# Optimization experiments

Hardware: AMD Instinct MI355X
Metric: run time of the kernel (lower is better)

Reference implementation:

```python
import jax, jax.numpy as jnp
import numpy as np

H, W = 2048, 2048          # frame size (cascade_size)
CS = 227                   # classifier_size
K = 16                     # max components classified per frame (fixed budget)
NC = 4                     # num_classes
THRESH = 0.5               # binarization threshold
MIN_SIZE = 64              # min component pixel count
CC_ITERS = 64              # label-propagation iterations for connected components


def _conv(x, w, stride=1, padding='SAME'):
    return jax.lax.conv_general_dilated(x, w, (stride, stride), padding,
                                        dimension_numbers=('NCHW', 'OIHW', 'NCHW'))


def _cascade(x, w1, w2, w3):
    # stand-in for Unet_plus(1,1): full-res segmentation head -> sigmoid mask
    h = jax.nn.relu(_conv(x, w1))
    h = jax.nn.relu(_conv(h, w2))
    return jax.nn.sigmoid(_conv(h, w3))   # [1,1,H,W]


def _classifier(roi, cw1, cw2, fc):
    # stand-in for CompactNet: roi [B,1,CS,CS] -> logits [B,NC]
    h = jax.nn.relu(_conv(roi, cw1, stride=4, padding='VALID'))
    h = jax.nn.relu(_conv(h, cw2, stride=2, padding='VALID'))
    g = h.mean(axis=(2, 3))               # global average pool -> [B,32]
    return g @ fc


def _connected_components(mask):
    # GPU-style min-index label propagation, 4-connectivity; background label = H*W
    BIG = H * W
    lab = jnp.where(mask, jnp.arange(BIG, dtype=jnp.int32).reshape(H, W), BIG)
    def step(_, lab):
        p = jnp.pad(lab, 1, constant_values=BIG)
        nmin = jnp.minimum(jnp.minimum(p[:-2, 1:-1], p[2:, 1:-1]),
                           jnp.minimum(p[1:-1, :-2], p[1:-1, 2:]))
        return jnp.where(mask, jnp.minimum(lab, nmin), BIG)
    return jax.lax.fori_loop(0, CC_ITERS, step, lab)


def _roi_resize(img, y0, y1, x0, x1):
    # bilinear warp of axis-aligned box [y0:y1, x0:x1] to CS x CS
    t = jnp.linspace(0.0, 1.0, CS)
    gy = y0.astype(jnp.float32) + t * (y1 - y0).astype(jnp.float32)
    gx = x0.astype(jnp.float32) + t * (x1 - x0).astype(jnp.float32)
    yf = jnp.clip(jnp.floor(gy).astype(jnp.int32), 0, H - 2)
    xf = jnp.clip(jnp.floor(gx).astype(jnp.int32), 0, W - 2)
    fy = (gy - yf)[:, None]
    fx = (gx - xf)[None, :]
    v00 = img[yf[:, None], xf[None, :]]
    v01 = img[yf[:, None], (xf + 1)[None, :]]
    v10 = img[(yf + 1)[:, None], xf[None, :]]
    v11 = img[(yf + 1)[:, None], (xf + 1)[None, :]]
    return (1 - fy) * ((1 - fx) * v00 + fx * v01) + fy * ((1 - fx) * v10 + fx * v11)


def _detect(x, w1, w2, w3, cw1, cw2, fc):
    pred_mask = _cascade(x, w1, w2, w3)[0, 0]          # [H,W]
    img = x[0, 0]
    mask = pred_mask > THRESH
    lab = jax.lax.stop_gradient(_connected_components(mask))
    counts = jnp.zeros(H * W + 1, jnp.int32).at[lab.ravel()].add(1)
    counts = counts.at[H * W].set(0)                   # drop background
    cnts, lids = jax.lax.top_k(counts, K)              # K largest components

    def per_comp(lid, cnt):
        cm = lab == lid                                # [H,W] component mask
        valid = (cnt >= MIN_SIZE)
        rowany = cm.any(axis=1)
        colany = cm.any(axis=0)
        y0 = jnp.argmax(rowany); y1 = H - 1 - jnp.argmax(rowany[::-1])
        x0 = jnp.argmax(colany); x1 = W - 1 - jnp.argmax(colany[::-1])
        roi = _roi_resize(img, y0, y1, x0, x1)         # [CS,CS] warped crop
        logits = _classifier(roi[None, None], cw1, cw2, fc)[0]
        return logits, cm, valid

    logits, cms, valids = jax.vmap(per_comp)(lids, cnts)   # [K,NC],[K,H,W],[K]
    return logits, cms, valids


def reference(x, w1, w2, w3, cw1, cw2, fc):
    logits, cms, valids = _detect(x, w1, w2, w3, cw1, cw2, fc)
    onehot = jax.nn.one_hot(jnp.argmax(logits, axis=1), NC) * valids[:, None]
    masks = jnp.einsum('kc,khw->chw', onehot, cms.astype(jnp.float32))
    return jnp.clip(masks, 0.0, 1.0)                   # [NC,H,W] per-class masks


def setup_inputs():
    key = jax.random.key(0)
    ks = jax.random.split(key, 7)
    def nrm(k, shape, fan_in):
        return jax.random.normal(k, shape, jnp.float32) / np.sqrt(fan_in).astype(np.float32)
    return {
        'x':   jax.random.normal(ks[0], (1, 1, H, W), jnp.float32),
        'w1':  nrm(ks[1], (32, 1, 3, 3), 9),
        'w2':  nrm(ks[2], (32, 32, 3, 3), 288),
        'w3':  nrm(ks[3], (1, 32, 1, 1), 32),
        'cw1': nrm(ks[4], (16, 1, 7, 7), 49),
        'cw2': nrm(ks[5], (32, 16, 3, 3), 144),
        'fc':  nrm(ks[6], (32, NC), 32),
    }
```

## Files before the change

### kernel.cpp

```cpp
#include <hip/hip_runtime.h>

#define HH 2048
#define WW 2048
#define HWTOT 4194304
#define BIGL 4194304
#define CSZ 227
#define NCLS 4
#define MINSZ 64
#define TF 1.1920928955078125e-7f
#define EPSB 5e-3f
#define LISTCAP 4000000

#define OFF_LABA 0u
#define OFF_LABB (1u<<24)
#define OFF_H1C  ((1u<<24) + 3538944u)
#define OFF_H2C  ((1u<<24) + 7077888u)
#define OFF_CAND ((1u<<24) + 9437184u)
#define OFF_CAND16 ((1u<<24) + 9437184u + 524288u)
#define OFF_COUNTS (2u<<24)
#define OFF_W2R  ((3u<<24) + 4096u)
#define OFF_LIST ((3u<<24) + 131072u)

typedef __attribute__((ext_vector_type(8))) short bf16x8;
typedef __attribute__((ext_vector_type(4))) float f32x4;
typedef unsigned int uint;
typedef unsigned short ushort;
typedef unsigned long long u64;

struct Meta {
  int lids[16];
  int valid[16];
  int cls[16];
  int bby0[16], bby1[16], bbx0[16], bbx1[16];
};

__device__ __forceinline__ ushort f2bf(float f) {
  uint u = __float_as_uint(f);
  u += 0x7fffu + ((u >> 16) & 1u);
  return (ushort)(u >> 16);
}
__device__ __forceinline__ float bf2f(ushort h) {
  return __uint_as_float(((uint)h) << 16);
}

#define HSWZ(px, g) ((px) * 32 + ((((g) ^ ((px) & 3))) << 3))

__global__ __launch_bounds__(256) void prep_kernel(const float* __restrict__ w2,
                                                   ushort* __restrict__ wfrag) {
  int i = blockIdx.x * 256 + threadIdx.x;
  if (i >= 18432) return;
  int fid = i >> 9, within = i & 511;
  int lane = within >> 3, j = within & 7;
  int tap = fid >> 2, m = (fid >> 1) & 1, p = fid & 1;
  int row = lane & 15, kgrp = lane >> 4;
  int ci = kgrp * 8 + j, oc = m * 16 + row;
  float w = w2[oc * 288 + ci * 9 + tap];
  ushort hb = f2bf(w);
  ushort val = hb;
  if (p) { float lof = w - bf2f(hb); val = f2bf(lof); }
  wfrag[i] = val;
}

__global__ __launch_bounds__(256) void cascade_kernel(
    const float* __restrict__ x, const float* __restrict__ w1,
    const ushort* __restrict__ wfrag, const float* __restrict__ w3,
    int* __restrict__ lab, int* __restrict__ list, int* __restrict__ list_count) {
  __shared__ float xs[12][36];
  __shared__ __align__(16) short hbuf[2][10880];

  const int tid = threadIdx.x;
  const int ox = blockIdx.x * 32, oy = blockIdx.y * 8;

  for (int i = tid; i < 432; i += 256) {
    int r = i / 36, c = i - r * 36;
    int gy = oy - 2 + r, gx = ox - 2 + c;
    float v = 0.f;
    if ((unsigned)gy < (unsigned)HH && (unsigned)gx < (unsigned)WW) v = x[gy * WW + gx];
    xs[r][c] = v;
  }
  __syncthreads();

  for (int px = tid; px < 340; px += 256) {
    const int hr = px / 34, hc = px - hr * 34;
    const int gy = oy - 1 + hr, gx = ox - 1 + hc;
    const bool inimg = ((unsigned)gy < (unsigned)HH) && ((unsigned)gx < (unsigned)WW);
    float a9[9];
#pragma unroll
    for (int du = 0; du < 3; ++du)
#pragma unroll
      for (int dv = 0; dv < 3; ++dv) a9[du * 3 + dv] = xs[hr + du][hc + dv];
#pragma unroll 1
    for (int g = 0; g < 4; ++g) {
      float sv[8];
#pragma unroll
      for (int cj = 0; cj < 8; ++cj) {
        const int ci = g * 8 + cj;
        float s = 0.f;
#pragma unroll
        for (int t = 0; t < 9; ++t) s = fmaf(a9[t], w1[ci * 9 + t], s);
        sv[cj] = inimg ? fmaxf(s, 0.f) : 0.f;
      }
      uint hp[4], lp[4];
#pragma unroll
      for (int q = 0; q < 4; ++q) {
        float s0 = sv[2 * q], s1 = sv[2 * q + 1];
        uint h2u;
        asm("v_cvt_pk_bf16_f32 %0, %1, %2" : "=v"(h2u) : "v"(s0), "v"(s1));
        float h0 = __uint_as_float(h2u << 16);
        float h1 = __uint_as_float(h2u & 0xffff0000u);
        uint l2u;
        asm("v_cvt_pk_bf16_f32 %0, %1, %2" : "=v"(l2u) : "v"(s0 - h0), "v"(s1 - h1));
        hp[q] = h2u; lp[q] = l2u;
      }
      *(int4*)&hbuf[0][HSWZ(px, g)] = make_int4(hp[0], hp[1], hp[2], hp[3]);
      *(int4*)&hbuf[1][HSWZ(px, g)] = make_int4(lp[0], lp[1], lp[2], lp[3]);
    }
  }
  __syncthreads();

  const int wv = tid >> 6, lane = tid & 63;
  const int col = lane & 15, kg = lane >> 4;
  const f32x4 zero4 = {0.f, 0.f, 0.f, 0.f};
  f32x4 acc[4][2];
#pragma unroll
  for (int i = 0; i < 4; ++i) { acc[i][0] = zero4; acc[i][1] = zero4; }

  const int4* wf4 = (const int4*)wfrag;
#pragma unroll 3
  for (int tap = 0; tap < 9; ++tap) {
    const int ty = tap / 3, tx = tap - ty * 3;
    bf16x8 a[2][2];
#pragma unroll
    for (int m = 0; m < 2; ++m)
#pragma unroll
      for (int p = 0; p < 2; ++p)
        a[m][p] = __builtin_bit_cast(bf16x8, wf4[(tap * 4 + m * 2 + p) * 64 + lane]);
#pragma unroll
    for (int ni = 0; ni < 4; ++ni) {
      const int nt = wv * 4 + ni;
      const int px = ((nt >> 1) + ty) * 34 + (nt & 1) * 16 + tx + col;
      bf16x8 bh = __builtin_bit_cast(bf16x8, *(const int4*)&hbuf[0][HSWZ(px, kg)]);
      bf16x8 bl = __builtin_bit_cast(bf16x8, *(const int4*)&hbuf[1][HSWZ(px, kg)]);
      acc[ni][0] = __builtin_amdgcn_mfma_f32_16x16x32_bf16(a[0][0], bh, acc[ni][0], 0, 0, 0);
      acc[ni][1] = __builtin_amdgcn_mfma_f32_16x16x32_bf16(a[1][0], bh, acc[ni][1], 0, 0, 0);
      acc[ni][0] = __builtin_amdgcn_mfma_f32_16x16x32_bf16(a[0][1], bh, acc[ni][0], 0, 0, 0);
      acc[ni][1] = __builtin_amdgcn_mfma_f32_16x16x32_bf16(a[1][1], bh, acc[ni][1], 0, 0, 0);
      acc[ni][0] = __builtin_amdgcn_mfma_f32_16x16x32_bf16(a[0][0], bl, acc[ni][0], 0, 0, 0);
      acc[ni][1] = __builtin_amdgcn_mfma_f32_16x16x32_bf16(a[1][0], bl, acc[ni][1], 0, 0, 0);
    }
  }

#pragma unroll 1
  for (int ni = 0; ni < 4; ++ni) {
    const int nt = wv * 4 + ni;
    float z = 0.f;
#pragma unroll
    for (int m = 0; m < 2; ++m)
#pragma unroll
      for (int r = 0; r < 4; ++r)
        z = fmaf(w3[m * 16 + kg * 4 + r], fmaxf(acc[ni][m][r], 0.f), z);
    z += __shfl_xor(z, 16);
    z += __shfl_xor(z, 32);
    const int gy = oy + (nt >> 1), gx = ox + (nt & 1) * 16 + col;
    const int p = gy * WW + gx;
    const bool act = lane < 16;
    if (act) lab[p] = (z > TF) ? p : BIGL;
    bool need = act && (fabsf(z - TF) < EPSB);
    unsigned long long mms = __ballot(need);
    if (mms) {
      int cnt = __popcll(mms);
      int prefix = __popcll(mms & ((1ull << lane) - 1ull));
      int basei = 0;
      if (need && prefix == 0) basei = atomicAdd(list_count, cnt);
      int srcl = __ffsll((long long)mms) - 1;
      basei = __shfl(basei, srcl);
      if (need && basei + prefix < LISTCAP) list[basei + prefix] = p;
    }
  }
}

__global__ __launch_bounds__(256) void recheck_kernel(
    const float* __restrict__ x, const float* __restrict__ w1,
    const float* __restrict__ w2, const float* __restrict__ w3,
    const int* __restrict__ list, const int* __restrict__ list_count,
    int* __restrict__ lab) {
  int n = *list_count;
  if (n > LISTCAP) n = LISTCAP;
  const int half = threadIdx.x & 1;
  for (int i = (blockIdx.x * 256 + threadIdx.x) >> 1; i < n; i += (2048 * 256) >> 1) {
    int p = list[i];
    int py = p >> 11, px = p & 2047;
    float xv[5][5];
#pragma unroll
    for (int u = 0; u < 5; ++u)
#pragma unroll
      for (int v = 0; v < 5; ++v) {
        int gy = py - 2 + u, gx = px - 2 + v;
        xv[u][v] = ((unsigned)gy < (unsigned)HH && (unsigned)gx < (unsigned)WW)
                       ? x[gy * WW + gx] : 0.f;
      }
    double acc2[32];
#pragma unroll
    for (int j = 0; j < 32; ++j) acc2[j] = 0.0;
    const int ci0 = half * 16;
#pragma unroll 1
    for (int ci = ci0; ci < ci0 + 16; ++ci) {
      float h1v[3][3];
#pragma unroll
      for (int u = 0; u < 3; ++u)
#pragma unroll
        for (int v = 0; v < 3; ++v) {
          int gy = py - 1 + u, gx = px - 1 + v;
          float s = 0.f;
#pragma unroll
          for (int t9 = 0; t9 < 9; ++t9)
            s = fmaf(xv[u + t9 / 3][v + t9 % 3], w1[ci * 9 + t9], s);
          bool inb = ((unsigned)gy < (unsigned)HH) && ((unsigned)gx < (unsigned)WW);
          h1v[u][v] = (inb && (s > 0.f)) ? s : 0.f;
        }
#pragma unroll
      for (int dy = 0; dy < 3; ++dy)
#pragma unroll
        for (int dx = 0; dx < 3; ++dx) {
          double hd = (double)h1v[dy][dx];
#pragma unroll
          for (int j = 0; j < 32; ++j)
            acc2[j] = fma(hd, (double)w2[j * 288 + ci * 9 + dy * 3 + dx], acc2[j]);
        }
    }
    double zz = 0.0;
#pragma unroll
    for (int j = 0; j < 32; ++j) {
      double other = __shfl_xor(acc2[j], 1);
      double tot = (half == 0) ? (acc2[j] + other) : (other + acc2[j]);
      zz = fma((double)w3[j], tot > 0.0 ? tot : 0.0, zz);
    }
    if (half == 0) lab[p] = (zz > 1.1920928955078125e-7) ? p : BIGL;
  }
}

__global__ __launch_bounds__(256) void cc16_kernel(const int* __restrict__ in,
                                                   int* __restrict__ out) {
  __shared__ __align__(16) int edgeL[24][100];
  __shared__ __align__(16) int edgeR[24][100];
  __shared__ __align__(16) int4 vtop[8][25];
  __shared__ __align__(16) int4 vbot[8][25];
  const int tid = threadIdx.x;
  const int bx = blockIdx.x & 31, by = blockIdx.x >> 5;
  const int ox0 = bx * 64 - 16, oy0 = by * 64 - 16;
  const bool act = tid < 192;
  const int g = tid % 24, s = tid / 24;
  const int gx = ox0 + g * 4;
  const bool colin = ((unsigned)gx < (unsigned)WW);
  int4 c[12];
#pragma unroll
  for (int r = 0; r < 12; ++r) c[r] = make_int4(BIGL, BIGL, BIGL, BIGL);
  if (act && colin) {
#pragma unroll
    for (int r = 0; r < 12; ++r) {
      int gy = oy0 + s * 12 + r;
      if ((unsigned)gy < (unsigned)HH) c[r] = *(const int4*)(in + gy * WW + gx);
    }
  }
#pragma unroll 1
  for (int step = 0; step < 16; ++step) {
    if (act) {
      *(int4*)&edgeL[g][s * 12 + 0] = make_int4(c[0].x, c[1].x, c[2].x, c[3].x);
      *(int4*)&edgeL[g][s * 12 + 4] = make_int4(c[4].x, c[5].x, c[6].x, c[7].x);
      *(int4*)&edgeL[g][s * 12 + 8] = make_int4(c[8].x, c[9].x, c[10].x, c[11].x);
      *(int4*)&edgeR[g][s * 12 + 0] = make_int4(c[0].w, c[1].w, c[2].w, c[3].w);
      *(int4*)&edgeR[g][s * 12 + 4] = make_int4(c[4].w, c[5].w, c[6].w, c[7].w);
      *(int4*)&edgeR[g][s * 12 + 8] = make_int4(c[8].w, c[9].w, c[10].w, c[11].w);
      vtop[s][g] = c[0];
      vbot[s][g] = c[11];
    }
    __syncthreads();
    if (act) {
      int lf[12], rt[12];
      if (g > 0) {
        int4 a0 = *(const int4*)&edgeR[g - 1][s * 12 + 0];
        int4 a1 = *(const int4*)&edgeR[g - 1][s * 12 + 4];
        int4 a2 = *(const int4*)&edgeR[g - 1][s * 12 + 8];
        lf[0] = a0.x; lf[1] = a0.y; lf[2] = a0.z; lf[3] = a0.w;
        lf[4] = a1.x; lf[5] = a1.y; lf[6] = a1.z; lf[7] = a1.w;
        lf[8] = a2.x; lf[9] = a2.y; lf[10] = a2.z; lf[11] = a2.w;
      } else {
#pragma unroll
        for (int r = 0; r < 12; ++r) lf[r] = BIGL;
      }
      if (g < 23) {
        int4 a0 = *(const int4*)&edgeL[g + 1][s * 12 + 0];
        int4 a1 = *(const int4*)&edgeL[g + 1][s * 12 + 4];
        int4 a2 = *(const int4*)&edgeL[g + 1][s * 12 + 8];
        rt[0] = a0.x; rt[1] = a0.y; rt[2] = a0.z; rt[3] = a0.w;
        rt[4] = a1.x; rt[5] = a1.y; rt[6] = a1.z; rt[7] = a1.w;
        rt[8] = a2.x; rt[9] = a2.y; rt[10] = a2.z; rt[11] = a2.w;
      } else {
#pragma unroll
        for (int r = 0; r < 12; ++r) rt[r] = BIGL;
      }
      int4 prev = (s > 0) ? vbot[s - 1][g] : make_int4(BIGL, BIGL, BIGL, BIGL);
      int4 dnlast = (s < 7) ? vtop[s + 1][g] : make_int4(BIGL, BIGL, BIGL, BIGL);
#pragma unroll
      for (int r = 0; r < 12; ++r) {
        int4 cur = c[r];
        int4 d = (r < 11) ? c[r + 1] : dnlast;
        int4 nr;
        nr.x = (cur.x == BIGL) ? BIGL : min(min(cur.x, cur.y), min(min(prev.x, d.x), lf[r]));
        nr.y = (cur.y == BIGL) ? BIGL : min(min(cur.y, min(cur.x, cur.z)), min(prev.y, d.y));
        nr.z = (cur.z == BIGL) ? BIGL : min(min(cur.z, min(cur.y, cur.w)), min(prev.z, d.z));
        nr.w = (cur.w == BIGL) ? BIGL : min(min(cur.w, min(cur.z, rt[r])), min(prev.w, d.w));
        c[r] = nr;
        prev = cur;
      }
    }
    __syncthreads();
  }
  if (act && g >= 4 && g < 20) {
#pragma unroll
    for (int r = 0; r < 12; ++r) {
      int row = s * 12 + r;
      if (row >= 16 && row < 80) {
        int gy = oy0 + row;
        *(int4*)(out + gy * WW + gx) = c[r];
      }
    }
  }
}

__global__ __launch_bounds__(256) void hist_kernel(const int* __restrict__ lab,
                                                   int* __restrict__ counts) {
  __shared__ int hkey[4096];
  __shared__ int hval[4096];
  int tid = threadIdx.x;
  for (int i = tid; i < 4096; i += 256) { hkey[i] = -1; hval[i] = 0; }
  __syncthreads();
  int t = blockIdx.x * 256 + tid;
  int p = t * 8;
  int4 a = *(const int4*)(lab + p), b = *(const int4*)(lab + p + 4);
  int v[8] = {a.x, a.y, a.z, a.w, b.x, b.y, b.z, b.w};
  int prev = -1, run = 0;
#pragma unroll
  for (int j = 0; j < 8; ++j) {
    int l = v[j];
    if (l == prev) { run++; continue; }
    if (prev >= 0 && prev != BIGL) {
      unsigned hh = (((unsigned)prev * 2654435761u) >> 20) & 4095u;
      for (;;) {
        int k = atomicCAS(&hkey[hh], -1, prev);
        if (k == -1 || k == prev) { atomicAdd(&hval[hh], run); break; }
        hh = (hh + 1) & 4095u;
      }
    }
    prev = l; run = 1;
  }
  if (prev >= 0 && prev != BIGL) {
    unsigned hh = (((unsigned)prev * 2654435761u) >> 20) & 4095u;
    for (;;) {
      int k = atomicCAS(&hkey[hh], -1, prev);
      if (k == -1 || k == prev) { atomicAdd(&hval[hh], run); break; }
      hh = (hh + 1) & 4095u;
    }
  }
  __syncthreads();
  for (int i = tid; i < 4096; i += 256)
    if (hkey[i] >= 0) atomicAdd(&counts[hkey[i]], hval[i]);
}

__global__ __launch_bounds__(256) void cand_kernel(const int* __restrict__ counts,
                                                   int2* __restrict__ cand,
                                                   int* __restrict__ cand_count) {
  int i = blockIdx.x * 256 + threadIdx.x;
  int lane = threadIdx.x & 63;
  int c = (i < HWTOT) ? counts[i] : 0;
  bool hit = (c >= MINSZ);
  unsigned long long m = __ballot(hit);
  if (m) {
    int cnt = __popcll(m);
    int prefix = __popcll(m & ((1ull << lane) - 1ull));
    int base = 0;
    if (hit && prefix == 0) base = atomicAdd(cand_count, cnt);
    int srcl = __ffsll((long long)m) - 1;
    base = __shfl(base, srcl);
    if (hit && base + prefix < 65536) cand[base + prefix] = make_int2(c, i);
  }
}

__global__ __launch_bounds__(256) void top16a_kernel(const int2* __restrict__ cand,
                                                     const int* __restrict__ cand_count,
                                                     u64* __restrict__ cand16) {
  __shared__ u64 skey[256];
  int tid = threadIdx.x;
  int n = *cand_count;
  if (n > 65536) n = 65536;
  u64 prev = ~0ull;
  for (int r = 0; r < 16; ++r) {
    u64 best = 0ull;
    for (int i = blockIdx.x * 256 + tid; i < n; i += 32 * 256) {
      int2 cc = cand[i];
      u64 key = ((u64)(unsigned)cc.x << 32) | (unsigned)(BIGL - cc.y);
      if (key < prev && key > best) best = key;
    }
    skey[tid] = best;
    __syncthreads();
    for (int st = 128; st > 0; st >>= 1) {
      if (tid < st && skey[tid + st] > skey[tid]) skey[tid] = skey[tid + st];
      __syncthreads();
    }
    u64 blockbest = skey[0];
    if (tid == 0) cand16[blockIdx.x * 16 + r] = blockbest;
    prev = blockbest;
    __syncthreads();
  }
}

__global__ __launch_bounds__(256) void top16b_kernel(const u64* __restrict__ cand16,
                                                     Meta* __restrict__ meta) {
  __shared__ u64 skey[256];
  int tid = threadIdx.x;
  u64 k0 = cand16[tid], k1 = cand16[tid + 256];
  u64 prev = ~0ull;
  for (int r = 0; r < 16; ++r) {
    u64 best = 0ull;
    if (k0 < prev && k0 > best) best = k0;
    if (k1 < prev && k1 > best) best = k1;
    skey[tid] = best;
    __syncthreads();
    for (int st = 128; st > 0; st >>= 1) {
      if (tid < st && skey[tid + st] > skey[tid]) skey[tid] = skey[tid + st];
      __syncthreads();
    }
    u64 blockbest = skey[0];
    if (tid == 0) {
      if (blockbest > 0ull) {
        meta->lids[r] = BIGL - (int)(blockbest & 0xffffffffull);
        meta->valid[r] = 1;
      } else {
        meta->lids[r] = -1;
        meta->valid[r] = 0;
      }
    }
    prev = blockbest;
    __syncthreads();
  }
  if (tid < 16) {
    meta->bby0[tid] = HH; meta->bby1[tid] = -1;
    meta->bbx0[tid] = WW; meta->bbx1[tid] = -1;
    meta->cls[tid] = 0;
  }
}

__global__ __launch_bounds__(256) void bbox_kernel(const int* __restrict__ lab,
                                                   Meta* __restrict__ meta) {
  __shared__ int lid_s[16];
  __shared__ int by0[16], by1[16], bx0[16], bx1[16];
  int tid = threadIdx.x;
  if (tid < 16) {
    lid_s[tid] = meta->lids[tid];
    by0[tid] = HH; by1[tid] = -1; bx0[tid] = WW; bx1[tid] = -1;
  }
  __syncthreads();
  int t = blockIdx.x * 256 + tid;
  int p = t * 8;
  int y = p >> 11, xbase = p & 2047;
  int4 a = *(const int4*)(lab + p), b = *(const int4*)(lab + p + 4);
  int v[8] = {a.x, a.y, a.z, a.w, b.x, b.y, b.z, b.w};
  int prev = BIGL, kprev = -1, xs = 0, xe = 0;
#pragma unroll
  for (int j = 0; j < 8; ++j) {
    int l = v[j];
    if (l == prev) { xe = xbase + j; continue; }
    if (kprev >= 0) {
      atomicMin(&by0[kprev], y); atomicMax(&by1[kprev], y);
      atomicMin(&bx0[kprev], xs); atomicMax(&bx1[kprev], xe);
    }
    prev = l; xs = xe = xbase + j; kprev = -1;
    if (l != BIGL) {
      for (int k = 0; k < 16; ++k)
        if (lid_s[k] == l) { kprev = k; break; }
    }
  }
  if (kprev >= 0) {
    atomicMin(&by0[kprev], y); atomicMax(&by1[kprev], y);
    atomicMin(&bx0[kprev], xs); atomicMax(&bx1[kprev], xe);
  }
  __syncthreads();
  if (tid < 16 && by1[tid] >= 0) {
    atomicMin(&meta->bby0[tid], by0[tid]); atomicMax(&meta->bby1[tid], by1[tid]);
    atomicMin(&meta->bbx0[tid], bx0[tid]); atomicMax(&meta->bbx1[tid], bx1[tid]);
  }
}

__global__ __launch_bounds__(256) void cconv1_kernel(const float* __restrict__ img,
                                                     const float* __restrict__ cw1,
                                                     const Meta* __restrict__ meta,
                                                     float* __restrict__ h1c) {
  int k = blockIdx.y, oy = blockIdx.x;
  if (!meta->valid[k]) return;
  __shared__ float srow[7][CSZ];
  float y0 = (float)meta->bby0[k], y1 = (float)meta->bby1[k];
  float x0 = (float)meta->bbx0[k], x1 = (float)meta->bbx1[k];
  for (int idx = threadIdx.x; idx < 7 * CSZ; idx += 256) {
    int rr = idx / CSZ, j = idx - rr * CSZ;
    int i = oy * 4 + rr;
    float ti = (float)i / 226.f, tj = (float)j / 226.f;
    float gy = y0 + ti * (y1 - y0);
    float gx = x0 + tj * (x1 - x0);
    int yf = (int)floorf(gy); yf = yf < 0 ? 0 : (yf > HH - 2 ? HH - 2 : yf);
    int xf = (int)floorf(gx); xf = xf < 0 ? 0 : (xf > WW - 2 ? WW - 2 : xf);
    float fy = gy - (float)yf, fx = gx - (float)xf;
    const float* r0 = img + yf * WW + xf;
    float v00 = r0[0], v01 = r0[1], v10 = r0[WW], v11 = r0[WW + 1];
    srow[rr][j] = (1.f - fy) * ((1.f - fx) * v00 + fx * v01) +
                  fy * ((1.f - fx) * v10 + fx * v11);
  }
  __syncthreads();
  for (int idx = threadIdx.x; idx < 16 * 56; idx += 256) {
    int ch = idx / 56, ox = idx - ch * 56;
    const float* wp = cw1 + ch * 49;
    float s = 0.f;
#pragma unroll
    for (int dy = 0; dy < 7; ++dy)
#pragma unroll
      for (int dx = 0; dx < 7; ++dx)
        s += srow[dy][ox * 4 + dx] * wp[dy * 7 + dx];
    h1c[((k * 16 + ch) * 56 + oy) * 56 + ox] = s > 0.f ? s : 0.f;
  }
}

__global__ __launch_bounds__(256) void cconv2_kernel(const float* __restrict__ h1c,
                                                     const float* __restrict__ cw2,
                                                     const Meta* __restrict__ meta,
                                                     float* __restrict__ h2c) {
  int k = blockIdx.y, oy = blockIdx.x;
  if (!meta->valid[k]) return;
  for (int idx = threadIdx.x; idx < 32 * 27; idx += 256) {
    int ch = idx / 27, ox = idx - ch * 27;
    float s = 0.f;
    for (int ci = 0; ci < 16; ++ci) {
      const float* hp = h1c + ((k * 16 + ci) * 56 + oy * 2) * 56 + ox * 2;
      const float* wp = cw2 + (ch * 16 + ci) * 9;
#pragma unroll
      for (int dy = 0; dy < 3; ++dy)
#pragma unroll
        for (int dx = 0; dx < 3; ++dx) s += hp[dy * 56 + dx] * wp[dy * 3 + dx];
    }
    h2c[((k * 32 + ch) * 27 + oy) * 27 + ox] = s > 0.f ? s : 0.f;
  }
}

__global__ __launch_bounds__(256) void poolfc_kernel(const float* __restrict__ h2c,
                                                     const float* __restrict__ fc,
                                                     Meta* __restrict__ meta) {
  int k = blockIdx.x;
  if (!meta->valid[k]) return;
  __shared__ float sums[8][32];
  int tid = threadIdx.x;
  int c = tid & 31, part = tid >> 5;
  float s = 0.f;
  const float* hp = h2c + (k * 32 + c) * 729;
  for (int j = part; j < 729; j += 8) s += hp[j];
  sums[part][c] = s;
  __syncthreads();
  if (tid < 32) {
    float g = 0.f;
#pragma unroll
    for (int p2 = 0; p2 < 8; ++p2) g += sums[p2][tid];
    sums[0][tid] = g / 729.f;
  }
  __syncthreads();
  if (tid == 0) {
    float best = -1e30f;
    int bi = 0;
    for (int j = 0; j < NCLS; ++j) {
      float lg = 0.f;
      for (int c2 = 0; c2 < 32; ++c2) lg += sums[0][c2] * fc[c2 * NCLS + j];
      if (lg > best) { best = lg; bi = j; }
    }
    meta->cls[k] = bi;
  }
}

__global__ __launch_bounds__(256) void final_kernel(const float* labf,
                                                    const Meta* __restrict__ meta,
                                                    float* out) {
  __shared__ int lid_s[16];
  __shared__ int cls_s[16];
  int tid = threadIdx.x;
  if (tid < 16) {
    lid_s[tid] = meta->valid[tid] ? meta->lids[tid] : -1;
    cls_s[tid] = meta->cls[tid];
  }
  __syncthreads();
  int t = blockIdx.x * 256 + tid;
  int p = t * 4;
  float4 lf = *(const float4*)(labf + p);
  int l4[4] = {__float_as_int(lf.x), __float_as_int(lf.y), __float_as_int(lf.z),
               __float_as_int(lf.w)};
  int cj[4];
#pragma unroll
  for (int j = 0; j < 4; ++j) {
    cj[j] = -1;
    int l = l4[j];
    if (l != BIGL) {
      for (int k = 0; k < 16; ++k)
        if (lid_s[k] == l) { cj[j] = cls_s[k]; break; }
    }
  }
#pragma unroll
  for (int c = 0; c < 4; ++c) {
    float4 w4 = make_float4(cj[0] == c ? 1.f : 0.f, cj[1] == c ? 1.f : 0.f,
                            cj[2] == c ? 1.f : 0.f, cj[3] == c ? 1.f : 0.f);
    *(float4*)(out + (size_t)c * HWTOT + p) = w4;
  }
}

extern "C" void kernel_launch(void* const* d_in, const int* in_sizes, int n_in,
                              void* d_out, int out_size, void* d_ws, size_t ws_size,
                              hipStream_t stream) {
  const float* x = (const float*)d_in[0];
  const float* w1 = (const float*)d_in[1];
  const float* w2 = (const float*)d_in[2];
  const float* w3 = (const float*)d_in[3];
  const float* cw1 = (const float*)d_in[4];
  const float* cw2 = (const float*)d_in[5];
  const float* fc = (const float*)d_in[6];

  char* base = (char*)d_out;
  int* lab_a = (int*)(base + OFF_LABA);
  int* lab_b = (int*)(base + OFF_LABB);
  float* h1c = (float*)(base + OFF_H1C);
  float* h2c = (float*)(base + OFF_H2C);
  int2* cand = (int2*)(base + OFF_CAND);
  u64* cand16 = (u64*)(base + OFF_CAND16);
  int* counts = (int*)(base + OFF_COUNTS);
  ushort* wfrag = (ushort*)(base + OFF_W2R);
  int* list = (int*)(base + OFF_LIST);
  int* cand_count = (int*)d_ws;
  int* list_count = (int*)((char*)d_ws + 64);
  Meta* meta = (Meta*)((char*)d_ws + 256);

  hipMemsetAsync(counts, 0, (size_t)(HWTOT + 1) * sizeof(int), stream);
  hipMemsetAsync(d_ws, 0, 128, stream);

  prep_kernel<<<72, 256, 0, stream>>>(w2, wfrag);
  cascade_kernel<<<dim3(64, 256), 256, 0, stream>>>(x, w1, wfrag, w3, lab_a, list, list_count);
  recheck_kernel<<<2048, 256, 0, stream>>>(x, w1, w2, w3, list, list_count, lab_a);

  for (int l = 0; l < 4; ++l) {
    const int* src = (l & 1) ? lab_b : lab_a;
    int* dst = (l & 1) ? lab_a : lab_b;
    cc16_kernel<<<1024, 256, 0, stream>>>(src, dst);
  }

  hist_kernel<<<2048, 256, 0, stream>>>(lab_a, counts);
  cand_kernel<<<16384, 256, 0, stream>>>(counts, cand, cand_count);
  top16a_kernel<<<32, 256, 0, stream>>>(cand, cand_count, cand16);
  top16b_kernel<<<1, 256, 0, stream>>>(cand16, meta);
  bbox_kernel<<<2048, 256, 0, stream>>>(lab_a, meta);
  cconv1_kernel<<<dim3(56, 16), 256, 0, stream>>>(x, cw1, meta, h1c);
  cconv2_kernel<<<dim3(27, 16), 256, 0, stream>>>(h1c, cw2, meta, h2c);
  poolfc_kernel<<<16, 256, 0, stream>>>(h2c, fc, meta);
  final_kernel<<<4096, 256, 0, stream>>>((const float*)d_out, meta, (float*)d_out);
}
```

Measured before the change: 662.6 us.

## Fuse label histogram into last CC pass and split recheck across four lanes

The final connected-components pass now builds the per-label shared-memory hash histogram from its register-resident labels, so the separate hist kernel and its full re-read of the label map are gone. The recheck kernel splits the 32 output channels across four lanes instead of two, each computing all 32 input channels with 8 double accumulators. The results are combined with two xor-shuffles. The workspace memset is folded into prep_kernel. This trades one global pass and one launch for more shared memory and an extra sync in the last CC kernel, and for redundant layer-1 compute in recheck.

```diff
diff --git a/kernel.cpp b/kernel.cpp
--- a/kernel.cpp
+++ b/kernel.cpp
@@ -34,6 +34,13 @@
   int bby0[16], bby1[16], bbx0[16], bbx1[16];
 };
 
+struct CCShared {
+  int edgeL[24][100];
+  int edgeR[24][100];
+  int4 vtop[8][25];
+  int4 vbot[8][25];
+};
+
 __device__ __forceinline__ ushort f2bf(float f) {
   uint u = __float_as_uint(f);
   u += 0x7fffu + ((u >> 16) & 1u);
@@ -46,7 +53,9 @@
 #define HSWZ(px, g) ((px) * 32 + ((((g) ^ ((px) & 3))) << 3))
 
 __global__ __launch_bounds__(256) void prep_kernel(const float* __restrict__ w2,
-                                                   ushort* __restrict__ wfrag) {
+                                                   ushort* __restrict__ wfrag,
+                                                   int* __restrict__ ws) {
+  if (blockIdx.x == 0 && threadIdx.x < 32) ws[threadIdx.x] = 0;
   int i = blockIdx.x * 256 + threadIdx.x;
   if (i >= 18432) return;
   int fid = i >> 9, within = i & 511;
@@ -186,9 +195,9 @@
     int* __restrict__ lab) {
   int n = *list_count;
   if (n > LISTCAP) n = LISTCAP;
-  const int half = threadIdx.x & 1;
-  for (int i = (blockIdx.x * 256 + threadIdx.x) >> 1; i < n; i += (2048 * 256) >> 1) {
-    int p = list[i];
+  const int jg = threadIdx.x & 3;
+  for (int q = (blockIdx.x * 256 + threadIdx.x) >> 2; q < n; q += (2048 * 256) >> 2) {
+    int p = list[q];
     int py = p >> 11, px = p & 2047;
     float xv[5][5];
 #pragma unroll
@@ -199,12 +208,11 @@
         xv[u][v] = ((unsigned)gy < (unsigned)HH && (unsigned)gx < (unsigned)WW)
                        ? x[gy * WW + gx] : 0.f;
       }
-    double acc2[32];
-#pragma unroll
-    for (int j = 0; j < 32; ++j) acc2[j] = 0.0;
-    const int ci0 = half * 16;
+    double acc2[8];
+#pragma unroll
+    for (int j = 0; j < 8; ++j) acc2[j] = 0.0;
 #pragma unroll 1
-    for (int ci = ci0; ci < ci0 + 16; ++ci) {
+    for (int ci = 0; ci < 32; ++ci) {
       float h1v[3][3];
 #pragma unroll
       for (int u = 0; u < 3; ++u)
@@ -224,27 +232,36 @@
         for (int dx = 0; dx < 3; ++dx) {
           double hd = (double)h1v[dy][dx];
 #pragma unroll
-          for (int j = 0; j < 32; ++j)
-            acc2[j] = fma(hd, (double)w2[j * 288 + ci * 9 + dy * 3 + dx], acc2[j]);
+          for (int j = 0; j < 8; ++j)
+            acc2[j] = fma(hd, (double)w2[(jg * 8 + j) * 288 + ci * 9 + dy * 3 + dx],
+                          acc2[j]);
         }
     }
     double zz = 0.0;
 #pragma unroll
-    for (int j = 0; j < 32; ++j) {
-      double other = __shfl_xor(acc2[j], 1);
-      double tot = (half == 0) ? (acc2[j] + other) : (other + acc2[j]);
-      zz = fma((double)w3[j], tot > 0.0 ? tot : 0.0, zz);
-    }
-    if (half == 0) lab[p] = (zz > 1.1920928955078125e-7) ? p : BIGL;
-  }
-}
-
+    for (int j = 0; j < 8; ++j)
+      zz = fma((double)w3[jg * 8 + j], acc2[j] > 0.0 ? acc2[j] : 0.0, zz);
+    zz += __shfl_xor(zz, 1);
+    zz += __shfl_xor(zz, 2);
+    if (jg == 0) lab[p] = (zz > 1.1920928955078125e-7) ? p : BIGL;
+  }
+}
+
+__device__ __forceinline__ void hist_add(int* hkey, int* hval, int label, int run) {
+  unsigned hh = (((unsigned)label * 2654435761u) >> 20) & 4095u;
+  for (;;) {
+    int k = atomicCAS(&hkey[hh], -1, label);
+    if (k == -1 || k == label) { atomicAdd(&hval[hh], run); break; }
+    hh = (hh + 1) & 4095u;
+  }
+}
+
+template <int DOHIST>
 __global__ __launch_bounds__(256) void cc16_kernel(const int* __restrict__ in,
-                                                   int* __restrict__ out) {
-  __shared__ __align__(16) int edgeL[24][100];
-  __shared__ __align__(16) int edgeR[24][100];
-  __shared__ __align__(16) int4 vtop[8][25];
-  __shared__ __align__(16) int4 vbot[8][25];
+                                                   int* __restrict__ out,
+                                                   int* __restrict__ counts) {
+  __shared__ __align__(16) char smem[32768];
+  CCShared* S = (CCShared*)smem;
   const int tid = threadIdx.x;
   const int bx = blockIdx.x & 31, by = blockIdx.x >> 5;
   const int ox0 = bx * 64 - 16, oy0 = by * 64 - 16;
@@ -265,22 +282,22 @@
 #pragma unroll 1
   for (int step = 0; step < 16; ++step) {
     if (act) {
-      *(int4*)&edgeL[g][s * 12 + 0] = make_int4(c[0].x, c[1].x, c[2].x, c[3].x);
-      *(int4*)&edgeL[g][s * 12 + 4] = make_int4(c[4].x, c[5].x, c[6].x, c[7].x);
-      *(int4*)&edgeL[g][s * 12 + 8] = make_int4(c[8].x, c[9].x, c[10].x, c[11].x);
-      *(int4*)&edgeR[g][s * 12 + 0] = make_int4(c[0].w, c[1].w, c[2].w, c[3].w);
-      *(int4*)&edgeR[g][s * 12 + 4] = make_int4(c[4].w, c[5].w, c[6].w, c[7].w);
-      *(int4*)&edgeR[g][s * 12 + 8] = make_int4(c[8].w, c[9].w, c[10].w, c[11].w);
-      vtop[s][g] = c[0];
-      vbot[s][g] = c[11];
+      *(int4*)&S->edgeL[g][s * 12 + 0] = make_int4(c[0].x, c[1].x, c[2].x, c[3].x);
+      *(int4*)&S->edgeL[g][s * 12 + 4] = make_int4(c[4].x, c[5].x, c[6].x, c[7].x);
+      *(int4*)&S->edgeL[g][s * 12 + 8] = make_int4(c[8].x, c[9].x, c[10].x, c[11].x);
+      *(int4*)&S->edgeR[g][s * 12 + 0] = make_int4(c[0].w, c[1].w, c[2].w, c[3].w);
+      *(int4*)&S->edgeR[g][s * 12 + 4] = make_int4(c[4].w, c[5].w, c[6].w, c[7].w);
+      *(int4*)&S->edgeR[g][s * 12 + 8] = make_int4(c[8].w, c[9].w, c[10].w, c[11].w);
+      S->vtop[s][g] = c[0];
+      S->vbot[s][g] = c[11];
     }
     __syncthreads();
     if (act) {
       int lf[12], rt[12];
       if (g > 0) {
-        int4 a0 = *(const int4*)&edgeR[g - 1][s * 12 + 0];
-        int4 a1 = *(const int4*)&edgeR[g - 1][s * 12 + 4];
-        int4 a2 = *(const int4*)&edgeR[g - 1][s * 12 + 8];
+        int4 a0 = *(const int4*)&S->edgeR[g - 1][s * 12 + 0];
+        int4 a1 = *(const int4*)&S->edgeR[g - 1][s * 12 + 4];
+        int4 a2 = *(const int4*)&S->edgeR[g - 1][s * 12 + 8];
         lf[0] = a0.x; lf[1] = a0.y; lf[2] = a0.z; lf[3] = a0.w;
         lf[4] = a1.x; lf[5] = a1.y; lf[6] = a1.z; lf[7] = a1.w;
         lf[8] = a2.x; lf[9] = a2.y; lf[10] = a2.z; lf[11] = a2.w;
@@ -289,9 +306,9 @@
         for (int r = 0; r < 12; ++r) lf[r] = BIGL;
       }
       if (g < 23) {
-        int4 a0 = *(const int4*)&edgeL[g + 1][s * 12 + 0];
-        int4 a1 = *(const int4*)&edgeL[g + 1][s * 12 + 4];
-        int4 a2 = *(const int4*)&edgeL[g + 1][s * 12 + 8];
+        int4 a0 = *(const int4*)&S->edgeL[g + 1][s * 12 + 0];
+        int4 a1 = *(const int4*)&S->edgeL[g + 1][s * 12 + 4];
+        int4 a2 = *(const int4*)&S->edgeL[g + 1][s * 12 + 8];
         rt[0] = a0.x; rt[1] = a0.y; rt[2] = a0.z; rt[3] = a0.w;
         rt[4] = a1.x; rt[5] = a1.y; rt[6] = a1.z; rt[7] = a1.w;
         rt[8] = a2.x; rt[9] = a2.y; rt[10] = a2.z; rt[11] = a2.w;
@@ -299,8 +316,8 @@
 #pragma unroll
         for (int r = 0; r < 12; ++r) rt[r] = BIGL;
       }
-      int4 prev = (s > 0) ? vbot[s - 1][g] : make_int4(BIGL, BIGL, BIGL, BIGL);
-      int4 dnlast = (s < 7) ? vtop[s + 1][g] : make_int4(BIGL, BIGL, BIGL, BIGL);
+      int4 prev = (s > 0) ? S->vbot[s - 1][g] : make_int4(BIGL, BIGL, BIGL, BIGL);
+      int4 dnlast = (s < 7) ? S->vtop[s + 1][g] : make_int4(BIGL, BIGL, BIGL, BIGL);
 #pragma unroll
       for (int r = 0; r < 12; ++r) {
         int4 cur = c[r];
@@ -316,6 +333,35 @@
     }
     __syncthreads();
   }
+
+  if (DOHIST) {
+    int* hkey = (int*)smem;
+    int* hval = (int*)(smem + 16384);
+    for (int i = tid; i < 4096; i += 256) { hkey[i] = -1; hval[i] = 0; }
+    __syncthreads();
+    if (act && g >= 4 && g < 20) {
+#pragma unroll 1
+      for (int r = 0; r < 12; ++r) {
+        int row = s * 12 + r;
+        if (row >= 16 && row < 80) {
+          int v[4] = {c[r].x, c[r].y, c[r].z, c[r].w};
+          int prev = -1, run = 0;
+#pragma unroll
+          for (int j = 0; j < 4; ++j) {
+            int l = v[j];
+            if (l == prev) { run++; continue; }
+            if (prev >= 0 && prev != BIGL) hist_add(hkey, hval, prev, run);
+            prev = l; run = 1;
+          }
+          if (prev >= 0 && prev != BIGL) hist_add(hkey, hval, prev, run);
+        }
+      }
+    }
+    __syncthreads();
+    for (int i = tid; i < 4096; i += 256)
+      if (hkey[i] >= 0) atomicAdd(&counts[hkey[i]], hval[i]);
+  }
+
   if (act && g >= 4 && g < 20) {
 #pragma unroll
     for (int r = 0; r < 12; ++r) {
@@ -326,45 +372,6 @@
       }
     }
   }
-}
-
-__global__ __launch_bounds__(256) void hist_kernel(const int* __restrict__ lab,
-                                                   int* __restrict__ counts) {
-  __shared__ int hkey[4096];
-  __shared__ int hval[4096];
-  int tid = threadIdx.x;
-  for (int i = tid; i < 4096; i += 256) { hkey[i] = -1; hval[i] = 0; }
-  __syncthreads();
-  int t = blockIdx.x * 256 + tid;
-  int p = t * 8;
-  int4 a = *(const int4*)(lab + p), b = *(const int4*)(lab + p + 4);
-  int v[8] = {a.x, a.y, a.z, a.w, b.x, b.y, b.z, b.w};
-  int prev = -1, run = 0;
-#pragma unroll
-  for (int j = 0; j < 8; ++j) {
-    int l = v[j];
-    if (l == prev) { run++; continue; }
-    if (prev >= 0 && prev != BIGL) {
-      unsigned hh = (((unsigned)prev * 2654435761u) >> 20) & 4095u;
-      for (;;) {
-        int k = atomicCAS(&hkey[hh], -1, prev);
-        if (k == -1 || k == prev) { atomicAdd(&hval[hh], run); break; }
-        hh = (hh + 1) & 4095u;
-      }
-    }
-    prev = l; run = 1;
-  }
-  if (prev >= 0 && prev != BIGL) {
-    unsigned hh = (((unsigned)prev * 2654435761u) >> 20) & 4095u;
-    for (;;) {
-      int k = atomicCAS(&hkey[hh], -1, prev);
-      if (k == -1 || k == prev) { atomicAdd(&hval[hh], run); break; }
-      hh = (hh + 1) & 4095u;
-    }
-  }
-  __syncthreads();
-  for (int i = tid; i < 4096; i += 256)
-    if (hkey[i] >= 0) atomicAdd(&counts[hkey[i]], hval[i]);
 }
 
 __global__ __launch_bounds__(256) void cand_kernel(const int* __restrict__ counts,
@@ -641,19 +648,17 @@
   Meta* meta = (Meta*)((char*)d_ws + 256);
 
   hipMemsetAsync(counts, 0, (size_t)(HWTOT + 1) * sizeof(int), stream);
-  hipMemsetAsync(d_ws, 0, 128, stream);
-
-  prep_kernel<<<72, 256, 0, stream>>>(w2, wfrag);
-  cascade_kernel<<<dim3(64, 256), 256, 0, stream>>>(x, w1, wfrag, w3, lab_a, list, list_count);
+
+  prep_kernel<<<72, 256, 0, stream>>>(w2, wfrag, (int*)d_ws);
+  cascade_kernel<<<dim3(64, 256), 256, 0, stream>>>(x, w1, wfrag, w3, lab_a, list,
+                                                    list_count);
   recheck_kernel<<<2048, 256, 0, stream>>>(x, w1, w2, w3, list, list_count, lab_a);
 
-  for (int l = 0; l < 4; ++l) {
-    const int* src = (l & 1) ? lab_b : lab_a;
-    int* dst = (l & 1) ? lab_a : lab_b;
-    cc16_kernel<<<1024, 256, 0, stream>>>(src, dst);
-  }
-
-  hist_kernel<<<2048, 256, 0, stream>>>(lab_a, counts);
+  cc16_kernel<0><<<1024, 256, 0, stream>>>(lab_a, lab_b, counts);
+  cc16_kernel<0><<<1024, 256, 0, stream>>>(lab_b, lab_a, counts);
+  cc16_kernel<0><<<1024, 256, 0, stream>>>(lab_a, lab_b, counts);
+  cc16_kernel<1><<<1024, 256, 0, stream>>>(lab_b, lab_a, counts);
+
   cand_kernel<<<16384, 256, 0, stream>>>(counts, cand, cand_count);
   top16a_kernel<<<32, 256, 0, stream>>>(cand, cand_count, cand16);
   top16b_kernel<<<1, 256, 0, stream>>>(cand16, meta);
```

New measurement: 811.5 us. 22.5% more time.
